# Performance work log

Hardware: AMD Instinct MI355X
Metric: run time of the kernel (lower is better)

The kernel has to match this reference:

```python
import jax, jax.numpy as jnp
import numpy as np

EPS = 1e-12  # torch F.normalize default eps

def l2norm(h):
    # torch.nn.functional.normalize(h, dim=1): x / max(||x||_2, eps)
    n = jnp.sqrt(jnp.sum(h * h, axis=1, keepdims=True))
    return h / jnp.maximum(n, EPS)

def setup_inputs() -> dict:
    key = jax.random.key(0)
    k1, k2, k3, k4, k5 = jax.random.split(key, 5)
    N, D, E, HOPS = 50000, 128, 600000, 3
    x = jax.random.normal(k1, (N, D), dtype=jnp.float32)
    edge_index = jax.random.randint(k2, (2, E), 0, N, dtype=jnp.int64)
    attn_w = jax.random.normal(k3, (HOPS, 2 * D), dtype=jnp.float32) * 0.05
    attn_b = jax.random.normal(k4, (HOPS,), dtype=jnp.float32) * 0.05
    noise = jax.random.normal(k5, (HOPS, N, D), dtype=jnp.float32)
    return {"x": x, "edge_index": edge_index, "attn_w": attn_w,
            "attn_b": attn_b, "noise": noise}

def reference(x, edge_index, attn_w, attn_b, noise):
    N = x.shape[0]
    sigma = 0.1
    src = edge_index[0]  # A[src, dst] = alpha; after transpose, aggr[dst] += alpha * h[src]
    dst = edge_index[1]
    outs = [l2norm(x)]
    num_hops = attn_w.shape[0]
    for k in range(num_hops):
        h = outs[-1]
        hs = h[src]                          # [E, D]
        hd = h[dst]                          # [E, D]
        # edge MLP: Linear(2D,1) + SELU, then sigmoid
        e = hs @ attn_w[k, : h.shape[1]] + hd @ attn_w[k, h.shape[1]:] + attn_b[k]  # [E]
        alpha = jax.nn.sigmoid(jax.nn.selu(e))  # [E]
        msg = alpha[:, None] * hs               # [E, D]
        aggr = jax.ops.segment_sum(msg, dst, num_segments=N)  # [N, D]
        noised = aggr + sigma * noise[k]
        outs.append(l2norm(noised))
    return jnp.stack(outs)  # [num_hops+1, N, D]
```

## Files before the change

### kernel.cpp

```cpp
#include <hip/hip_runtime.h>
#include <math.h>

#define EPSN 1e-12f

__device__ __forceinline__ float wave_sum(float v) {
#pragma unroll
  for (int o = 32; o >= 1; o >>= 1) v += __shfl_xor(v, o);
  return v;
}

__device__ __forceinline__ float edge_alpha(float e) {
  const float SC = 1.0507009873554805f;
  const float AL = 1.6732632423543772f;
  float se = e > 0.f ? SC * e : SC * AL * (__expf(e) - 1.f);
  return 1.f / (1.f + __expf(-se));
}

__global__ __launch_bounds__(256) void hist_kernel(const int* __restrict__ dst,
                                                   int* __restrict__ counts, int E) {
  int e = blockIdx.x * 256 + threadIdx.x;
  if (e < E) atomicAdd(&counts[dst[e]], 1);
}

__global__ __launch_bounds__(256) void scan_blocks(const int* __restrict__ counts,
                                                   int* __restrict__ offsets,
                                                   int* __restrict__ bsums, int n) {
  __shared__ int tmp[256];
  int tid = threadIdx.x, gid = blockIdx.x * 256 + tid;
  int v = (gid < n) ? counts[gid] : 0;
  tmp[tid] = v;
  __syncthreads();
  for (int o = 1; o < 256; o <<= 1) {
    int t = (tid >= o) ? tmp[tid - o] : 0;
    __syncthreads();
    tmp[tid] += t;
    __syncthreads();
  }
  if (gid < n) offsets[gid] = tmp[tid] - v;
  if (tid == 255) bsums[blockIdx.x] = tmp[255];
}

__global__ __launch_bounds__(256) void scan_bsums(int* bsums, int nb) {
  __shared__ int tmp[256];
  int tid = threadIdx.x;
  int v = (tid < nb) ? bsums[tid] : 0;
  tmp[tid] = v;
  __syncthreads();
  for (int o = 1; o < 256; o <<= 1) {
    int t = (tid >= o) ? tmp[tid - o] : 0;
    __syncthreads();
    tmp[tid] += t;
    __syncthreads();
  }
  if (tid < nb) bsums[tid] = tmp[tid] - v;
}

__global__ __launch_bounds__(256) void scan_add(int* offsets, const int* __restrict__ bsums, int n) {
  int gid = blockIdx.x * 256 + threadIdx.x;
  if (gid < n) offsets[gid] += bsums[blockIdx.x];
}

__global__ __launch_bounds__(256) void scatter_kernel(const int* __restrict__ ei,
                                                      const int* __restrict__ offsets,
                                                      int* cursor, int* __restrict__ src_sorted, int E) {
  int e = blockIdx.x * 256 + threadIdx.x;
  if (e < E) {
    int d = ei[E + e];
    int pos = atomicAdd(&cursor[d], 1);
    src_sorted[offsets[d] + pos] = ei[e];
  }
}

__global__ __launch_bounds__(256) void init_kernel(const float* __restrict__ x,
                                                   const float* __restrict__ attn_w,
                                                   float* __restrict__ out0,
                                                   float* __restrict__ p1, float* __restrict__ p2, int N) {
  int wid = (int)((blockIdx.x * blockDim.x + threadIdx.x) >> 6);
  int lane = threadIdx.x & 63;
  if (wid >= N) return;
  const float2* x2 = (const float2*)x;
  float2 v = x2[(size_t)wid * 64 + lane];
  float ss = wave_sum(v.x * v.x + v.y * v.y);
  float inv = 1.f / fmaxf(sqrtf(ss), EPSN);
  v.x *= inv; v.y *= inv;
  ((float2*)out0)[(size_t)wid * 64 + lane] = v;
  float d1 = wave_sum(v.x * attn_w[2 * lane] + v.y * attn_w[2 * lane + 1]);
  float d2 = wave_sum(v.x * attn_w[128 + 2 * lane] + v.y * attn_w[128 + 2 * lane + 1]);
  if (lane == 0) { p1[wid] = d1; p2[wid] = d2; }
}

__global__ __launch_bounds__(256) void hop_kernel(const float* __restrict__ h,
                                                  const float* __restrict__ p1,
                                                  const float* __restrict__ p2,
                                                  const int* __restrict__ offsets,
                                                  const int* __restrict__ counts,
                                                  const int* __restrict__ src_sorted,
                                                  const float* __restrict__ noise_k,
                                                  const float* __restrict__ attn_b, int k,
                                                  float* __restrict__ out_next,
                                                  float* __restrict__ np1, float* __restrict__ np2,
                                                  const float* __restrict__ wnext,
                                                  int N, int last) {
  int wid = (int)((blockIdx.x * blockDim.x + threadIdx.x) >> 6);
  int lane = threadIdx.x & 63;
  if (wid >= N) return;
  int start = offsets[wid];
  int cnt = counts[wid];
  float p2d = p2[wid] + attn_b[k];
  const float2* h2 = (const float2*)h;
  float a0 = 0.f, a1 = 0.f;

  for (int base = 0; base < cnt; base += 64) {
    int m = cnt - base; if (m > 64) m = 64;
    int idx = base + lane;
    int s_l = 0; float al_l = 0.f;
    if (idx < cnt) {
      s_l = src_sorted[start + idx];
      al_l = edge_alpha(p1[s_l] + p2d);
    }
    int j = 0;
    for (; j + 4 <= m; j += 4) {
      int s0 = __shfl(s_l, j), s1 = __shfl(s_l, j + 1);
      int s2 = __shfl(s_l, j + 2), s3 = __shfl(s_l, j + 3);
      float A0 = __shfl(al_l, j), A1 = __shfl(al_l, j + 1);
      float A2 = __shfl(al_l, j + 2), A3 = __shfl(al_l, j + 3);
      float2 v0 = h2[(size_t)s0 * 64 + lane];
      float2 v1 = h2[(size_t)s1 * 64 + lane];
      float2 v2 = h2[(size_t)s2 * 64 + lane];
      float2 v3 = h2[(size_t)s3 * 64 + lane];
      a0 += A0 * v0.x; a1 += A0 * v0.y;
      a0 += A1 * v1.x; a1 += A1 * v1.y;
      a0 += A2 * v2.x; a1 += A2 * v2.y;
      a0 += A3 * v3.x; a1 += A3 * v3.y;
    }
    for (; j < m; ++j) {
      int s = __shfl(s_l, j);
      float A = __shfl(al_l, j);
      float2 v = h2[(size_t)s * 64 + lane];
      a0 += A * v.x; a1 += A * v.y;
    }
  }

  float2 nz = ((const float2*)noise_k)[(size_t)wid * 64 + lane];
  a0 += 0.1f * nz.x;
  a1 += 0.1f * nz.y;
  float ss = wave_sum(a0 * a0 + a1 * a1);
  float inv = 1.f / fmaxf(sqrtf(ss), EPSN);
  a0 *= inv; a1 *= inv;
  float2 o; o.x = a0; o.y = a1;
  ((float2*)out_next)[(size_t)wid * 64 + lane] = o;
  if (!last) {
    float d1 = wave_sum(a0 * wnext[2 * lane] + a1 * wnext[2 * lane + 1]);
    float d2 = wave_sum(a0 * wnext[128 + 2 * lane] + a1 * wnext[128 + 2 * lane + 1]);
    if (lane == 0) { np1[wid] = d1; np2[wid] = d2; }
  }
}

extern "C" void kernel_launch(void* const* d_in, const int* in_sizes, int n_in,
                              void* d_out, int out_size, void* d_ws, size_t ws_size,
                              hipStream_t stream) {
  const float* x      = (const float*)d_in[0];
  const int*   ei     = (const int*)d_in[1];
  const float* attn_w = (const float*)d_in[2];
  const float* attn_b = (const float*)d_in[3];
  const float* noise  = (const float*)d_in[4];
  float* out = (float*)d_out;

  const int N = in_sizes[0] / 128;
  const int E = in_sizes[1] / 2;
  const int HOPS = in_sizes[3];

  auto align = [](size_t v) { return (v + 255) & ~size_t(255); };
  char* w = (char*)d_ws;
  int* counts     = (int*)w; w += align((size_t)N * 4);
  int* cursor     = (int*)w; w += align((size_t)N * 4);
  int* offsets    = (int*)w; w += align((size_t)N * 4);
  int* bsums      = (int*)w; w += align(1024);
  int* src_sorted = (int*)w; w += align((size_t)E * 4);
  float* pA1 = (float*)w; w += align((size_t)N * 4);
  float* pA2 = (float*)w; w += align((size_t)N * 4);
  float* pB1 = (float*)w; w += align((size_t)N * 4);
  float* pB2 = (float*)w; w += align((size_t)N * 4);

  hipMemsetAsync(counts, 0, (size_t)N * 4, stream);
  hipMemsetAsync(cursor, 0, (size_t)N * 4, stream);

  int ebl = (E + 255) / 256;
  int nbl = (N + 255) / 256;
  hist_kernel<<<ebl, 256, 0, stream>>>(ei + E, counts, E);
  scan_blocks<<<nbl, 256, 0, stream>>>(counts, offsets, bsums, N);
  scan_bsums<<<1, 256, 0, stream>>>(bsums, nbl);
  scan_add<<<nbl, 256, 0, stream>>>(offsets, bsums, N);
  scatter_kernel<<<ebl, 256, 0, stream>>>(ei, offsets, cursor, src_sorted, E);

  int wbl = (N + 3) / 4;
  init_kernel<<<wbl, 256, 0, stream>>>(x, attn_w, out, pA1, pA2, N);

  float* p1b[2] = {pA1, pB1};
  float* p2b[2] = {pA2, pB2};
  for (int k = 0; k < HOPS; ++k) {
    int cur = k & 1, nxt = cur ^ 1;
    int last = (k == HOPS - 1) ? 1 : 0;
    const float* wnext = last ? attn_w : (attn_w + (size_t)(k + 1) * 256);
    hop_kernel<<<wbl, 256, 0, stream>>>(out + (size_t)k * N * 128,
                                        p1b[cur], p2b[cur],
                                        offsets, counts, src_sorted,
                                        noise + (size_t)k * N * 128, attn_b, k,
                                        out + (size_t)(k + 1) * N * 128,
                                        p1b[nxt], p2b[nxt], wnext,
                                        N, last);
  }
}
```

Measured before the change: 390.1 us.

## Gather neighbor features from fp16 shadow copy and use nontemporal streaming I/O

Each hop now writes a half-precision copy of the normalized features and gathers neighbor rows from it, which halves the bytes per random gather. Output and noise traffic uses nontemporal loads and stores so these streams do not pollute cache. The CSR scatter also seeds its cursor with the offsets, which drops a memset and an offsets load per edge. Accumulating from fp16 inputs adds rounding error that may exceed the tolerance.

Result: faster. 362.7 us (-7.0%).

```diff
diff --git a/kernel.cpp b/kernel.cpp
--- a/kernel.cpp
+++ b/kernel.cpp
@@ -1,4 +1,5 @@
 #include <hip/hip_runtime.h>
+#include <hip/hip_fp16.h>
 #include <math.h>
 
 #define EPSN 1e-12f
@@ -55,25 +56,30 @@
   if (tid < nb) bsums[tid] = tmp[tid] - v;
 }
 
-__global__ __launch_bounds__(256) void scan_add(int* offsets, const int* __restrict__ bsums, int n) {
+__global__ __launch_bounds__(256) void scan_add(int* offsets, int* cursor,
+                                                const int* __restrict__ bsums, int n) {
   int gid = blockIdx.x * 256 + threadIdx.x;
-  if (gid < n) offsets[gid] += bsums[blockIdx.x];
+  if (gid < n) {
+    int v = offsets[gid] + bsums[blockIdx.x];
+    offsets[gid] = v;
+    cursor[gid] = v;
+  }
 }
 
 __global__ __launch_bounds__(256) void scatter_kernel(const int* __restrict__ ei,
-                                                      const int* __restrict__ offsets,
                                                       int* cursor, int* __restrict__ src_sorted, int E) {
   int e = blockIdx.x * 256 + threadIdx.x;
   if (e < E) {
     int d = ei[E + e];
     int pos = atomicAdd(&cursor[d], 1);
-    src_sorted[offsets[d] + pos] = ei[e];
+    src_sorted[pos] = ei[e];
   }
 }
 
 __global__ __launch_bounds__(256) void init_kernel(const float* __restrict__ x,
                                                    const float* __restrict__ attn_w,
                                                    float* __restrict__ out0,
+                                                   __half2* __restrict__ hb0,
                                                    float* __restrict__ p1, float* __restrict__ p2, int N) {
   int wid = (int)((blockIdx.x * blockDim.x + threadIdx.x) >> 6);
   int lane = threadIdx.x & 63;
@@ -83,13 +89,16 @@
   float ss = wave_sum(v.x * v.x + v.y * v.y);
   float inv = 1.f / fmaxf(sqrtf(ss), EPSN);
   v.x *= inv; v.y *= inv;
-  ((float2*)out0)[(size_t)wid * 64 + lane] = v;
+  float* op = out0 + (size_t)wid * 128 + lane * 2;
+  __builtin_nontemporal_store(v.x, op);
+  __builtin_nontemporal_store(v.y, op + 1);
+  hb0[(size_t)wid * 64 + lane] = __floats2half2_rn(v.x, v.y);
   float d1 = wave_sum(v.x * attn_w[2 * lane] + v.y * attn_w[2 * lane + 1]);
   float d2 = wave_sum(v.x * attn_w[128 + 2 * lane] + v.y * attn_w[128 + 2 * lane + 1]);
   if (lane == 0) { p1[wid] = d1; p2[wid] = d2; }
 }
 
-__global__ __launch_bounds__(256) void hop_kernel(const float* __restrict__ h,
+__global__ __launch_bounds__(256) void hop_kernel(const __half2* __restrict__ hb,
                                                   const float* __restrict__ p1,
                                                   const float* __restrict__ p2,
                                                   const int* __restrict__ offsets,
@@ -98,6 +107,7 @@
                                                   const float* __restrict__ noise_k,
                                                   const float* __restrict__ attn_b, int k,
                                                   float* __restrict__ out_next,
+                                                  __half2* __restrict__ hb_next,
                                                   float* __restrict__ np1, float* __restrict__ np2,
                                                   const float* __restrict__ wnext,
                                                   int N, int last) {
@@ -107,7 +117,6 @@
   int start = offsets[wid];
   int cnt = counts[wid];
   float p2d = p2[wid] + attn_b[k];
-  const float2* h2 = (const float2*)h;
   float a0 = 0.f, a1 = 0.f;
 
   for (int base = 0; base < cnt; base += 64) {
@@ -124,10 +133,10 @@
       int s2 = __shfl(s_l, j + 2), s3 = __shfl(s_l, j + 3);
       float A0 = __shfl(al_l, j), A1 = __shfl(al_l, j + 1);
       float A2 = __shfl(al_l, j + 2), A3 = __shfl(al_l, j + 3);
-      float2 v0 = h2[(size_t)s0 * 64 + lane];
-      float2 v1 = h2[(size_t)s1 * 64 + lane];
-      float2 v2 = h2[(size_t)s2 * 64 + lane];
-      float2 v3 = h2[(size_t)s3 * 64 + lane];
+      float2 v0 = __half22float2(hb[(size_t)s0 * 64 + lane]);
+      float2 v1 = __half22float2(hb[(size_t)s1 * 64 + lane]);
+      float2 v2 = __half22float2(hb[(size_t)s2 * 64 + lane]);
+      float2 v3 = __half22float2(hb[(size_t)s3 * 64 + lane]);
       a0 += A0 * v0.x; a1 += A0 * v0.y;
       a0 += A1 * v1.x; a1 += A1 * v1.y;
       a0 += A2 * v2.x; a1 += A2 * v2.y;
@@ -136,20 +145,22 @@
     for (; j < m; ++j) {
       int s = __shfl(s_l, j);
       float A = __shfl(al_l, j);
-      float2 v = h2[(size_t)s * 64 + lane];
+      float2 v = __half22float2(hb[(size_t)s * 64 + lane]);
       a0 += A * v.x; a1 += A * v.y;
     }
   }
 
-  float2 nz = ((const float2*)noise_k)[(size_t)wid * 64 + lane];
-  a0 += 0.1f * nz.x;
-  a1 += 0.1f * nz.y;
+  const float* nr = noise_k + (size_t)wid * 128 + lane * 2;
+  a0 += 0.1f * __builtin_nontemporal_load(nr);
+  a1 += 0.1f * __builtin_nontemporal_load(nr + 1);
   float ss = wave_sum(a0 * a0 + a1 * a1);
   float inv = 1.f / fmaxf(sqrtf(ss), EPSN);
   a0 *= inv; a1 *= inv;
-  float2 o; o.x = a0; o.y = a1;
-  ((float2*)out_next)[(size_t)wid * 64 + lane] = o;
+  float* op = out_next + (size_t)wid * 128 + lane * 2;
+  __builtin_nontemporal_store(a0, op);
+  __builtin_nontemporal_store(a1, op + 1);
   if (!last) {
+    hb_next[(size_t)wid * 64 + lane] = __floats2half2_rn(a0, a1);
     float d1 = wave_sum(a0 * wnext[2 * lane] + a1 * wnext[2 * lane + 1]);
     float d2 = wave_sum(a0 * wnext[128 + 2 * lane] + a1 * wnext[128 + 2 * lane + 1]);
     if (lane == 0) { np1[wid] = d1; np2[wid] = d2; }
@@ -181,32 +192,35 @@
   float* pA2 = (float*)w; w += align((size_t)N * 4);
   float* pB1 = (float*)w; w += align((size_t)N * 4);
   float* pB2 = (float*)w; w += align((size_t)N * 4);
+  __half2* hbA = (__half2*)w; w += align((size_t)N * 64 * 4);
+  __half2* hbB = (__half2*)w; w += align((size_t)N * 64 * 4);
 
   hipMemsetAsync(counts, 0, (size_t)N * 4, stream);
-  hipMemsetAsync(cursor, 0, (size_t)N * 4, stream);
 
   int ebl = (E + 255) / 256;
   int nbl = (N + 255) / 256;
   hist_kernel<<<ebl, 256, 0, stream>>>(ei + E, counts, E);
   scan_blocks<<<nbl, 256, 0, stream>>>(counts, offsets, bsums, N);
   scan_bsums<<<1, 256, 0, stream>>>(bsums, nbl);
-  scan_add<<<nbl, 256, 0, stream>>>(offsets, bsums, N);
-  scatter_kernel<<<ebl, 256, 0, stream>>>(ei, offsets, cursor, src_sorted, E);
+  scan_add<<<nbl, 256, 0, stream>>>(offsets, cursor, bsums, N);
+  scatter_kernel<<<ebl, 256, 0, stream>>>(ei, cursor, src_sorted, E);
 
   int wbl = (N + 3) / 4;
-  init_kernel<<<wbl, 256, 0, stream>>>(x, attn_w, out, pA1, pA2, N);
+  init_kernel<<<wbl, 256, 0, stream>>>(x, attn_w, out, hbA, pA1, pA2, N);
 
   float* p1b[2] = {pA1, pB1};
   float* p2b[2] = {pA2, pB2};
+  __half2* hbb[2] = {hbA, hbB};
   for (int k = 0; k < HOPS; ++k) {
     int cur = k & 1, nxt = cur ^ 1;
     int last = (k == HOPS - 1) ? 1 : 0;
     const float* wnext = last ? attn_w : (attn_w + (size_t)(k + 1) * 256);
-    hop_kernel<<<wbl, 256, 0, stream>>>(out + (size_t)k * N * 128,
+    hop_kernel<<<wbl, 256, 0, stream>>>(hbb[cur],
                                         p1b[cur], p2b[cur],
                                         offsets, counts, src_sorted,
                                         noise + (size_t)k * N * 128, attn_b, k,
                                         out + (size_t)(k + 1) * N * 128,
+                                        hbb[nxt],
                                         p1b[nxt], p2b[nxt], wnext,
                                         N, last);
   }
```
